# Kernel optimization log

Hardware: AMD Instinct MI355X
Metric: run time of the kernel (lower is better)

The kernel has to match this reference:

```python
import jax, jax.numpy as jnp
import numpy as np


def _layernorm(x, g, b, eps=1e-5):
    mu = jnp.mean(x, axis=-1, keepdims=True)
    var = jnp.mean(jnp.square(x - mu), axis=-1, keepdims=True)
    return (x - mu) * jax.lax.rsqrt(var + eps) * g + b


def setup_inputs() -> dict:
    key = jax.random.key(0)
    ks = jax.random.split(key, 8)
    dim, ctx_dim, heads, dim_head = 256, 256, 8, 64
    inner = heads * dim_head
    s = 0.02
    return {
        "x": jax.random.normal(ks[0], (4, dim, 64, 64), jnp.float32),
        "y": jax.random.normal(ks[1], (4, 1024, ctx_dim), jnp.float32),
        "ln_x_g": jnp.ones((dim,), jnp.float32),
        "ln_x_b": jnp.zeros((dim,), jnp.float32),
        "ln_y_g": jnp.ones((ctx_dim,), jnp.float32),
        "ln_y_b": jnp.zeros((ctx_dim,), jnp.float32),
        "Wq": jax.random.normal(ks[2], (dim, inner), jnp.float32) * s,
        "Wk": jax.random.normal(ks[3], (ctx_dim, inner), jnp.float32) * s,
        "Wv": jax.random.normal(ks[4], (ctx_dim, inner), jnp.float32) * s,
        "bv": jnp.zeros((inner,), jnp.float32),
        "Wo": jax.random.normal(ks[5], (inner, dim), jnp.float32) * s,
        "bo": jnp.zeros((dim,), jnp.float32),
    }


def reference(x, y, ln_x_g, ln_x_b, ln_y_g, ln_y_b, Wq, Wk, Wv, bv, Wo, bo):
    heads, dim_head = 8, 64
    b, c = x.shape[:2]
    # channel_last=False path: [b, c, H, W] -> [b, n, c]
    xn = x.reshape(b, c, -1).swapaxes(1, 2)
    xn = _layernorm(xn, ln_x_g, ln_x_b)          # note: x is reassigned in torch code
    yn = _layernorm(y, ln_y_g, ln_y_b)
    q = xn @ Wq                                   # [b, n, h*d]
    k = yn @ Wk                                   # [b, m, h*d]
    v = yn @ Wv + bv                              # [b, m, h*d]

    def split_heads(t):
        B, N, _ = t.shape
        return t.reshape(B, N, heads, dim_head).transpose(0, 2, 1, 3)  # [b, h, n, d]

    q, k, v = split_heads(q), split_heads(k), split_heads(v)
    attn = jnp.einsum("bhid,bhjd->bhij", q, k) * (dim_head ** -0.5)
    attn = jax.nn.softmax(attn, axis=-1)
    out = jnp.einsum("bhij,bhjd->bhid", attn, v)  # [b, h, n, d]
    out = out.transpose(0, 2, 1, 3).reshape(b, -1, heads * dim_head)
    out = out @ Wo + bo
    return xn + out  # residual with layernormed x (faithful to source)
```

## Files before the change

kernel.cpp:

```cpp
#include <hip/hip_runtime.h>
#include <hip/hip_bf16.h>
#include <cstddef>
#include <cstdint>

#define BATCH 4
#define CDIM 256
#define HW 4096
#define MCTX 1024
#define CTX 256
#define HEADS 8
#define DHEAD 64
#define INNER 512

typedef __attribute__((ext_vector_type(8))) short bf16x8;
typedef __attribute__((ext_vector_type(4))) float f32x4;
typedef __attribute__((ext_vector_type(16))) float f32x16;

static __device__ __forceinline__ ushort f2bf(float f) {
  __hip_bfloat16 h = __float2bfloat16(f);
  return *reinterpret_cast<ushort*>(&h);
}

static __device__ __forceinline__ void gload16(const void* g, void* l) {
  __builtin_amdgcn_global_load_lds(
      (const __attribute__((address_space(1))) void*)(uintptr_t)g,
      (__attribute__((address_space(3))) void*)(uint32_t)(uintptr_t)l,
      16, 0, 0);
}

static __device__ __forceinline__ void ln_x_body(
    const float* __restrict__ x, const float* __restrict__ g,
    const float* __restrict__ bta, float* __restrict__ xn,
    ushort* __restrict__ xnbf, int blk) {
  const int bi = blk / (HW / 32);
  const int n0 = (blk % (HW / 32)) * 32;
  __shared__ float xt[32][257];
  __shared__ float smu[32], srs[32];
  const int t = threadIdx.x;
  const float* xb = x + (size_t)bi * CDIM * HW;
  {
    const int cr = t >> 3;
    const int n4 = (t & 7) * 4;
    #pragma unroll
    for (int pass = 0; pass < 8; ++pass) {
      const int c = pass * 32 + cr;
      float4 v = *(const float4*)(xb + (size_t)c * HW + n0 + n4);
      xt[n4 + 0][c] = v.x; xt[n4 + 1][c] = v.y;
      xt[n4 + 2][c] = v.z; xt[n4 + 3][c] = v.w;
    }
  }
  __syncthreads();
  const int col = t >> 3, j = t & 7;
  float s = 0.f, ss = 0.f;
  #pragma unroll
  for (int c = j; c < CDIM; c += 8) {
    float v = xt[col][c];
    s += v; ss += v * v;
  }
  #pragma unroll
  for (int off = 1; off < 8; off <<= 1) {
    s += __shfl_xor(s, off);
    ss += __shfl_xor(ss, off);
  }
  if (j == 0) {
    float mu = s * (1.f / CDIM);
    smu[col] = mu;
    srs[col] = rsqrtf(ss * (1.f / CDIM) - mu * mu + 1e-5f);
  }
  __syncthreads();
  const float gv = g[t], bvv = bta[t];
  float* xnb = xn + ((size_t)bi * HW + n0) * CDIM;
  ushort* xbb = xnbf + ((size_t)bi * HW + n0) * CDIM;
  #pragma unroll 4
  for (int n = 0; n < 32; ++n) {
    float val = (xt[n][t] - smu[n]) * srs[n] * gv + bvv;
    xnb[(size_t)n * CDIM + t] = val;
    xbb[(size_t)n * CDIM + t] = f2bf(val);
  }
}

static __device__ __forceinline__ void ln_y_body(
    const float* __restrict__ y, const float* __restrict__ g,
    const float* __restrict__ bta, ushort* __restrict__ ynbf, int blk) {
  const int row = blk * 4 + (threadIdx.x >> 6);
  const int t = threadIdx.x & 63;
  float4 v = ((const float4*)(y + (size_t)row * CTX))[t];
  float s = v.x + v.y + v.z + v.w;
  float ss = v.x * v.x + v.y * v.y + v.z * v.z + v.w * v.w;
  #pragma unroll
  for (int off = 1; off < 64; off <<= 1) {
    s += __shfl_xor(s, off);
    ss += __shfl_xor(ss, off);
  }
  float mu = s * (1.f / CTX);
  float rs = rsqrtf(ss * (1.f / CTX) - mu * mu + 1e-5f);
  float4 gv = ((const float4*)g)[t];
  float4 b4 = ((const float4*)bta)[t];
  ushort4 ob;
  ob.x = f2bf((v.x - mu) * rs * gv.x + b4.x);
  ob.y = f2bf((v.y - mu) * rs * gv.y + b4.y);
  ob.z = f2bf((v.z - mu) * rs * gv.z + b4.z);
  ob.w = f2bf((v.w - mu) * rs * gv.w + b4.w);
  *(ushort4*)(ynbf + (size_t)row * CTX + t * 4) = ob;
}

static __device__ __forceinline__ void wprep_body(
    const float* __restrict__ W, ushort* __restrict__ Wt, int K, int N,
    int bx, int by) {
  __shared__ ushort T[64][65];
  const int k0 = by * 64, n0 = bx * 64;
  const int t = threadIdx.x;
  #pragma unroll
  for (int rr = 0; rr < 4; ++rr) {
    int row = rr * 16 + (t >> 4);
    int c = (t & 15) * 4;
    float4 wv = *(const float4*)(W + (size_t)(k0 + row) * N + n0 + c);
    T[row][c + 0] = f2bf(wv.x); T[row][c + 1] = f2bf(wv.y);
    T[row][c + 2] = f2bf(wv.z); T[row][c + 3] = f2bf(wv.w);
  }
  __syncthreads();
  #pragma unroll
  for (int rr = 0; rr < 4; ++rr) {
    int nrow = rr * 16 + (t >> 4);
    int kc = (t & 15) * 4;
    ushort4 o;
    o.x = T[kc + 0][nrow]; o.y = T[kc + 1][nrow];
    o.z = T[kc + 2][nrow]; o.w = T[kc + 3][nrow];
    *(ushort4*)(Wt + (size_t)(n0 + nrow) * K + k0 + kc) = o;
  }
}

__global__ __launch_bounds__(256) void prep_kernel(
    const float* __restrict__ x, const float* __restrict__ ln_xg,
    const float* __restrict__ ln_xb, float* __restrict__ xn,
    ushort* __restrict__ xnbf,
    const float* __restrict__ y, const float* __restrict__ ln_yg,
    const float* __restrict__ ln_yb, ushort* __restrict__ ynbf,
    const float* __restrict__ Wq, const float* __restrict__ Wk,
    const float* __restrict__ Wv, const float* __restrict__ Wo,
    ushort* __restrict__ wtq, ushort* __restrict__ wtk,
    ushort* __restrict__ wtv, ushort* __restrict__ wto) {
  const int id = blockIdx.x;
  if (id < 512) {
    ln_x_body(x, ln_xg, ln_xb, xn, xnbf, id);
  } else if (id < 1536) {
    ln_y_body(y, ln_yg, ln_yb, ynbf, id - 512);
  } else {
    const int r = id - 1536;
    const int z = r >> 5, rem = r & 31;
    const int bx = rem & 7, by = rem >> 3;
    if (z < 3) {
      const float* W = (z == 0) ? Wq : (z == 1) ? Wk : Wv;
      ushort* Wt = (z == 0) ? wtq : (z == 1) ? wtk : wtv;
      wprep_body(W, Wt, 256, 512, bx, by);
    } else {
      wprep_body(Wo, wto, 512, 256, bx & 3, by * 2 + (bx >> 2));
    }
  }
}

template <bool F32_RES_OUT>
static __device__ __forceinline__ void gemm_body(
    const ushort* __restrict__ A, const ushort* __restrict__ Bt,
    const float* __restrict__ bias, const float* __restrict__ res,
    void* __restrict__ Cout, ushort* __restrict__ vt_out,
    int M, int N, int K, float scale, int m0, int n0) {
  __shared__ ushort As[128 * 64];
  __shared__ ushort Bs[128 * 64];
  const int t = threadIdx.x;
  const int l = t & 63, w = t >> 6;
  const int lq = l & 15, lg = l >> 4;
  const int wr = w >> 1, wc = w & 1;
  f32x4 acc[4][4];
  #pragma unroll
  for (int mt = 0; mt < 4; ++mt)
    #pragma unroll
    for (int nt = 0; nt < 4; ++nt)
      #pragma unroll
      for (int e = 0; e < 4; ++e) acc[mt][nt][e] = 0.f;
  const int srow = w * 8 + (l >> 3);
  const int scol = ((l & 7) ^ (l >> 3)) * 8;
  const ushort* pA = A + (size_t)(m0 + srow) * K + scol;
  const ushort* pB = Bt + (size_t)(n0 + srow) * K + scol;
  const int dbase = w * 512;
  for (int k0 = 0; k0 < K; k0 += 64) {
    if (k0) __syncthreads();
    #pragma unroll
    for (int i = 0; i < 4; ++i) {
      gload16(pA + (size_t)(i * 32) * K + k0, &As[i * 2048 + dbase]);
      gload16(pB + (size_t)(i * 32) * K + k0, &Bs[i * 2048 + dbase]);
    }
    __syncthreads();
    #pragma unroll
    for (int ks = 0; ks < 2; ++ks) {
      bf16x8 af[4], bfr[4];
      #pragma unroll
      for (int mt = 0; mt < 4; ++mt) {
        const int R = wr * 64 + mt * 16 + lq;
        af[mt] = *(const bf16x8*)(
            &As[R * 64 + ((ks * 32 + lg * 8) ^ ((R & 7) * 8))]);
      }
      #pragma unroll
      for (int nt = 0; nt < 4; ++nt) {
        const int R = wc * 64 + nt * 16 + lq;
        bfr[nt] = *(const bf16x8*)(
            &Bs[R * 64 + ((ks * 32 + lg * 8) ^ ((R & 7) * 8))]);
      }
      #pragma unroll
      for (int mt = 0; mt < 4; ++mt)
        #pragma unroll
        for (int nt = 0; nt < 4; ++nt)
          acc[mt][nt] = __builtin_amdgcn_mfma_f32_16x16x32_bf16(
              af[mt], bfr[nt], acc[mt][nt], 0, 0, 0);
    }
  }
  #pragma unroll
  for (int nt = 0; nt < 4; ++nt) {
    const int colc = n0 + wc * 64 + nt * 16 + lq;
    const float bcol = bias ? bias[colc] : 0.f;
    #pragma unroll
    for (int mt = 0; mt < 4; ++mt) {
      #pragma unroll
      for (int i = 0; i < 4; ++i) {
        const size_t row = (size_t)(m0 + wr * 64 + mt * 16 + lg * 4 + i);
        float v = acc[mt][nt][i] * scale + bcol;
        if (vt_out) {
          vt_out[(size_t)((((row >> 10) * 8 + (colc >> 6)) << 6) + (colc & 63)) * MCTX
                 + (row & (MCTX - 1))] = f2bf(v);
        } else if (F32_RES_OUT) {
          ((float*)Cout)[row * N + colc] = v + res[row * N + colc];
        } else {
          ((ushort*)Cout)[row * N + colc] = f2bf(v);
        }
      }
    }
  }
}

__global__ __launch_bounds__(256) void qkv_kernel(
    const ushort* __restrict__ xnbf, const ushort* __restrict__ ynbf,
    const ushort* __restrict__ wtq, const ushort* __restrict__ wtk,
    const ushort* __restrict__ wtv, const float* __restrict__ bv,
    ushort* __restrict__ qbf, ushort* __restrict__ kbf,
    ushort* __restrict__ vtb) {
  const int id = blockIdx.x;
  if (id < 512) {
    gemm_body<false>(xnbf, wtq, nullptr, nullptr, qbf, nullptr,
                     16384, 512, 256, 0.1803368801111204f,
                     (id >> 2) * 128, (id & 3) * 128);
  } else if (id < 640) {
    const int i2 = id - 512;
    gemm_body<false>(ynbf, wtk, nullptr, nullptr, kbf, nullptr,
                     4096, 512, 256, 1.f, (i2 >> 2) * 128, (i2 & 3) * 128);
  } else {
    const int i2 = id - 640;
    gemm_body<false>(ynbf, wtv, bv, nullptr, nullptr, vtb,
                     4096, 512, 256, 1.f, (i2 >> 2) * 128, (i2 & 3) * 128);
  }
}

template <bool F32_RES_OUT>
__global__ __launch_bounds__(256) void mfma_gemm(
    const ushort* __restrict__ A, const ushort* __restrict__ Bt,
    const float* __restrict__ bias, const float* __restrict__ res,
    void* __restrict__ Cout, int M, int N, int K, float scale) {
  gemm_body<F32_RES_OUT>(A, Bt, bias, res, Cout, nullptr, M, N, K, scale,
                         blockIdx.y * 128, blockIdx.x * 128);
}

__global__ __launch_bounds__(512, 4) void attn_mfma(
    const ushort* __restrict__ q, const ushort* __restrict__ k,
    const ushort* __restrict__ vt, ushort* __restrict__ ao) {
  const int bid = blockIdx.x + 16 * (blockIdx.y + 8 * blockIdx.z);
  const int swz = (bid & 7) * 64 + (bid >> 3);
  const int bi = swz >> 7;
  const int h = (swz >> 4) & 7;
  const int n0 = (swz & 15) * 256;
  const int tile0 = (bid & 3) << 2;
  __shared__ ushort Ks[2][64 * 64];
  __shared__ ushort Vs[2][64 * 64];
  const int t = threadIdx.x;
  const int l = t & 63, w = t >> 6;
  const int lq32 = l & 31, hi = l >> 5;

  bf16x8 bq[4];
  {
    const size_t qrow = (size_t)(bi * HW + n0 + w * 32 + lq32);
    #pragma unroll
    for (int ds = 0; ds < 4; ++ds)
      bq[ds] = *(const bf16x8*)(q + qrow * INNER + h * DHEAD + ds * 16 + hi * 8);
  }

  float m_run = -1e30f, l_run = 0.f;
  f32x16 oacc[2];
  #pragma unroll
  for (int dt = 0; dt < 2; ++dt)
    #pragma unroll
    for (int e = 0; e < 16; ++e) oacc[dt][e] = 0.f;

  const int rr = t >> 3, cc = (t & 7) * 8;
  const ushort* kptr = k + (size_t)(bi * MCTX + rr) * INNER + h * DHEAD + cc;
  const ushort* vptr = vt + (size_t)((bi * HEADS + h) * 64 + rr) * MCTX + cc;
  const int sidx = (rr * 64 + cc) ^ ((rr & 7) << 3);

  {
    const int ms = tile0 << 6;
    uint4 k0v = *(const uint4*)(kptr + (size_t)ms * INNER);
    uint4 v0v = *(const uint4*)(vptr + ms);
    *(uint4*)(&Ks[0][sidx]) = k0v;
    *(uint4*)(&Vs[0][sidx]) = v0v;
  }
  __syncthreads();

  #pragma unroll 2
  for (int it = 0; it < 16; ++it) {
    const int buf = it & 1;
    const bool more = (it + 1) < 16;
    const int mnext = ((tile0 + it + 1) & 15) << 6;
    uint4 kpre{}, vpre{};
    if (more) {
      kpre = *(const uint4*)(kptr + (size_t)mnext * INNER);
      vpre = *(const uint4*)(vptr + mnext);
    }
    f32x16 sc[2];
    #pragma unroll
    for (int kt = 0; kt < 2; ++kt)
      #pragma unroll
      for (int e = 0; e < 16; ++e) sc[kt][e] = 0.f;
    __builtin_amdgcn_s_setprio(1);
    #pragma unroll
    for (int kt = 0; kt < 2; ++kt) {
      #pragma unroll
      for (int ds = 0; ds < 4; ++ds) {
        const int krow = kt * 32 + lq32;
        bf16x8 ak = *(const bf16x8*)(
            &Ks[buf][(krow * 64 + ds * 16 + hi * 8) ^ ((krow & 7) << 3)]);
        sc[kt] = __builtin_amdgcn_mfma_f32_32x32x16_bf16(ak, bq[ds], sc[kt], 0, 0, 0);
      }
    }
    __builtin_amdgcn_s_setprio(0);
    f32x16 mx;
    #pragma unroll
    for (int e = 0; e < 16; ++e) mx[e] = fmaxf(sc[0][e], sc[1][e]);
    #pragma unroll
    for (int e = 0; e < 8; ++e) mx[e] = fmaxf(mx[e], mx[e + 8]);
    #pragma unroll
    for (int e = 0; e < 4; ++e) mx[e] = fmaxf(mx[e], mx[e + 4]);
    float mloc = fmaxf(fmaxf(mx[0], mx[1]), fmaxf(mx[2], mx[3]));
    mloc = fmaxf(mloc, __shfl_xor(mloc, 32));
    if (!__all((int)(mloc - m_run <= 8.f))) {
      const float mnew = fmaxf(m_run, mloc);
      const float corr = __builtin_amdgcn_exp2f(m_run - mnew);
      l_run *= corr;
      m_run = mnew;
      #pragma unroll
      for (int r = 0; r < 16; ++r) {
        const int qrow = (r & 3) + 8 * (r >> 2) + 4 * hi;
        float ci = __shfl(corr, qrow);
        oacc[0][r] *= ci; oacc[1][r] *= ci;
      }
    }
    #pragma unroll
    for (int kt = 0; kt < 2; ++kt)
      #pragma unroll
      for (int e = 0; e < 16; ++e)
        sc[kt][e] = __builtin_amdgcn_exp2f(sc[kt][e] - m_run);
    f32x16 s16;
    #pragma unroll
    for (int e = 0; e < 16; ++e) s16[e] = sc[0][e] + sc[1][e];
    #pragma unroll
    for (int e = 0; e < 8; ++e) s16[e] += s16[e + 8];
    #pragma unroll
    for (int e = 0; e < 4; ++e) s16[e] += s16[e + 4];
    float psum = (s16[0] + s16[1]) + (s16[2] + s16[3]);
    psum += __shfl_xor(psum, 32);
    l_run += psum;
    bf16x8 pafr[4];
    #pragma unroll
    for (int kt = 0; kt < 2; ++kt) {
      uint wa[4], wb[4];
      #pragma unroll
      for (int r4 = 0; r4 < 4; ++r4) {
        wa[r4] = (uint)f2bf(sc[kt][4 * r4]) | ((uint)f2bf(sc[kt][4 * r4 + 1]) << 16);
        wb[r4] = (uint)f2bf(sc[kt][4 * r4 + 2]) | ((uint)f2bf(sc[kt][4 * r4 + 3]) << 16);
      }
      #pragma unroll
      for (int p2 = 0; p2 < 2; ++p2) {
        uint Sa = wa[2 * p2], Da = wa[2 * p2 + 1];
        uint Sb = wb[2 * p2], Db = wb[2 * p2 + 1];
        asm volatile("v_permlane32_swap_b32 %0, %1" : "+v"(Da), "+v"(Sa));
        asm volatile("v_permlane32_swap_b32 %0, %1" : "+v"(Db), "+v"(Sb));
        uint4 fr;
        fr.x = Sa; fr.y = Sb; fr.z = Da; fr.w = Db;
        pafr[kt * 2 + p2] = *reinterpret_cast<bf16x8*>(&fr);
      }
    }
    if (more) {
      *(uint4*)(&Ks[buf ^ 1][sidx]) = kpre;
      *(uint4*)(&Vs[buf ^ 1][sidx]) = vpre;
    }
    __builtin_amdgcn_s_setprio(1);
    #pragma unroll
    for (int dt = 0; dt < 2; ++dt) {
      const int vrow = dt * 32 + lq32;
      #pragma unroll
      for (int kt16 = 0; kt16 < 4; ++kt16) {
        bf16x8 vb = *(const bf16x8*)(
            &Vs[buf][(vrow * 64 + kt16 * 16 + hi * 8) ^ ((vrow & 7) << 3)]);
        oacc[dt] = __builtin_amdgcn_mfma_f32_32x32x16_bf16(pafr[kt16], vb, oacc[dt], 0, 0, 0);
      }
    }
    __builtin_amdgcn_s_setprio(0);
    __syncthreads();
  }
  const float rl = 1.f / l_run;
  #pragma unroll
  for (int r = 0; r < 16; ++r) {
    const int qrow = (r & 3) + 8 * (r >> 2) + 4 * hi;
    float li = __shfl(rl, qrow);
    const size_t row = (size_t)(bi * HW + n0 + w * 32 + qrow);
    ao[row * INNER + h * DHEAD + lq32] = f2bf(oacc[0][r] * li);
    ao[row * INNER + h * DHEAD + 32 + lq32] = f2bf(oacc[1][r] * li);
  }
}

extern "C" void kernel_launch(void* const* d_in, const int* in_sizes, int n_in,
                              void* d_out, int out_size, void* d_ws, size_t ws_size,
                              hipStream_t stream) {
  const float* x     = (const float*)d_in[0];
  const float* y     = (const float*)d_in[1];
  const float* ln_xg = (const float*)d_in[2];
  const float* ln_xb = (const float*)d_in[3];
  const float* ln_yg = (const float*)d_in[4];
  const float* ln_yb = (const float*)d_in[5];
  const float* Wq    = (const float*)d_in[6];
  const float* Wk    = (const float*)d_in[7];
  const float* Wv    = (const float*)d_in[8];
  const float* bv    = (const float*)d_in[9];
  const float* Wo    = (const float*)d_in[10];
  const float* bo    = (const float*)d_in[11];
  float* out = (float*)d_out;

  char* p = (char*)d_ws;
  float*  xn   = (float*)p;  p += (size_t)16384 * 256 * 4;
  ushort* xnbf = (ushort*)p; p += (size_t)16384 * 256 * 2;
  ushort* ynbf = (ushort*)p; p += (size_t)4096 * 256 * 2;
  ushort* wtq  = (ushort*)p; p += (size_t)512 * 256 * 2;
  ushort* wtk  = (ushort*)p; p += (size_t)512 * 256 * 2;
  ushort* wtv  = (ushort*)p; p += (size_t)512 * 256 * 2;
  ushort* wto  = (ushort*)p; p += (size_t)256 * 512 * 2;
  ushort* qbf  = (ushort*)p; p += (size_t)16384 * 512 * 2;
  ushort* kbf  = (ushort*)p; p += (size_t)4096 * 512 * 2;
  ushort* vtb  = (ushort*)p; p += (size_t)4096 * 512 * 2;
  ushort* aobf = (ushort*)p; p += (size_t)16384 * 512 * 2;

  prep_kernel<<<dim3(512 + 1024 + 128), 256, 0, stream>>>(
      x, ln_xg, ln_xb, xn, xnbf, y, ln_yg, ln_yb, ynbf,
      Wq, Wk, Wv, Wo, wtq, wtk, wtv, wto);
  qkv_kernel<<<dim3(768), 256, 0, stream>>>(
      xnbf, ynbf, wtq, wtk, wtv, bv, qbf, kbf, vtb);
  attn_mfma<<<dim3(HW / 256, HEADS, BATCH), 512, 0, stream>>>(qbf, kbf, vtb, aobf);
  mfma_gemm<true><<<dim3(2, 128), 256, 0, stream>>>(
      aobf, wto, bo, xn, out, 16384, 256, 512, 1.f);
}
```

Baseline: 104.3 us.

## Process two query tiles per attention wave and add dedicated 64-row output GEMM

The attention kernel now has each wave handle 64 query rows as two 32-row groups that share each K/V tile read from LDS. This halves the grid and the K/V global and LDS traffic per query, and the second group's softmax can overlap with the first group's MFMA work. The cost is roughly double the accumulator registers, so launch bounds drop from 4 to 2 blocks per SM. The output projection gets its own 64x128-tile kernel using 16x16x32 MFMAs, which doubles its block count for better occupancy on a narrow N=256 GEMM.

After: 105.3 us. Within noise of the previous version (+0.9%).

```diff
diff --git a/kernel.cpp b/kernel.cpp
--- a/kernel.cpp
+++ b/kernel.cpp
@@ -259,23 +259,84 @@
   }
 }
 
-template <bool F32_RES_OUT>
-__global__ __launch_bounds__(256) void mfma_gemm(
+__global__ __launch_bounds__(256) void ao_gemm_kernel(
     const ushort* __restrict__ A, const ushort* __restrict__ Bt,
     const float* __restrict__ bias, const float* __restrict__ res,
-    void* __restrict__ Cout, int M, int N, int K, float scale) {
-  gemm_body<F32_RES_OUT>(A, Bt, bias, res, Cout, nullptr, M, N, K, scale,
-                         blockIdx.y * 128, blockIdx.x * 128);
-}
-
-__global__ __launch_bounds__(512, 4) void attn_mfma(
+    float* __restrict__ out) {
+  __shared__ ushort As[64 * 64];
+  __shared__ ushort Bs[128 * 64];
+  const int t = threadIdx.x;
+  const int l = t & 63, w = t >> 6;
+  const int lq = l & 15, lg = l >> 4;
+  const int wr = w >> 1, wc = w & 1;
+  const int m0 = blockIdx.y * 64, n0 = blockIdx.x * 128;
+  f32x4 acc[2][4];
+  #pragma unroll
+  for (int mt = 0; mt < 2; ++mt)
+    #pragma unroll
+    for (int nt = 0; nt < 4; ++nt)
+      #pragma unroll
+      for (int e = 0; e < 4; ++e) acc[mt][nt][e] = 0.f;
+  const int srow = w * 8 + (l >> 3);
+  const int scol = ((l & 7) ^ (l >> 3)) * 8;
+  const ushort* pA = A + (size_t)(m0 + srow) * INNER + scol;
+  const ushort* pB = Bt + (size_t)(n0 + srow) * INNER + scol;
+  const int dbase = w * 512;
+  for (int k0 = 0; k0 < INNER; k0 += 64) {
+    if (k0) __syncthreads();
+    #pragma unroll
+    for (int i = 0; i < 2; ++i)
+      gload16(pA + (size_t)(i * 32) * INNER + k0, &As[i * 2048 + dbase]);
+    #pragma unroll
+    for (int i = 0; i < 4; ++i)
+      gload16(pB + (size_t)(i * 32) * INNER + k0, &Bs[i * 2048 + dbase]);
+    __syncthreads();
+    #pragma unroll
+    for (int ks = 0; ks < 2; ++ks) {
+      bf16x8 af[2], bfr[4];
+      #pragma unroll
+      for (int mt = 0; mt < 2; ++mt) {
+        const int R = wr * 32 + mt * 16 + lq;
+        af[mt] = *(const bf16x8*)(
+            &As[R * 64 + ((ks * 32 + lg * 8) ^ ((R & 7) * 8))]);
+      }
+      #pragma unroll
+      for (int nt = 0; nt < 4; ++nt) {
+        const int R = wc * 64 + nt * 16 + lq;
+        bfr[nt] = *(const bf16x8*)(
+            &Bs[R * 64 + ((ks * 32 + lg * 8) ^ ((R & 7) * 8))]);
+      }
+      #pragma unroll
+      for (int mt = 0; mt < 2; ++mt)
+        #pragma unroll
+        for (int nt = 0; nt < 4; ++nt)
+          acc[mt][nt] = __builtin_amdgcn_mfma_f32_16x16x32_bf16(
+              af[mt], bfr[nt], acc[mt][nt], 0, 0, 0);
+    }
+  }
+  #pragma unroll
+  for (int nt = 0; nt < 4; ++nt) {
+    const int colc = n0 + wc * 64 + nt * 16 + lq;
+    const float bcol = bias[colc];
+    #pragma unroll
+    for (int mt = 0; mt < 2; ++mt) {
+      #pragma unroll
+      for (int i = 0; i < 4; ++i) {
+        const size_t row = (size_t)(m0 + wr * 32 + mt * 16 + lg * 4 + i);
+        out[row * CDIM + colc] = acc[mt][nt][i] + bcol + res[row * CDIM + colc];
+      }
+    }
+  }
+}
+
+__global__ __launch_bounds__(512, 2) void attn_mfma(
     const ushort* __restrict__ q, const ushort* __restrict__ k,
     const ushort* __restrict__ vt, ushort* __restrict__ ao) {
-  const int bid = blockIdx.x + 16 * (blockIdx.y + 8 * blockIdx.z);
-  const int swz = (bid & 7) * 64 + (bid >> 3);
-  const int bi = swz >> 7;
-  const int h = (swz >> 4) & 7;
-  const int n0 = (swz & 15) * 256;
+  const int bid = blockIdx.x + 8 * (blockIdx.y + 8 * blockIdx.z);
+  const int swz = (bid & 7) * 32 + (bid >> 3);
+  const int bi = swz >> 6;
+  const int h = (swz >> 3) & 7;
+  const int n0 = (swz & 7) * 512;
   const int tile0 = (bid & 3) << 2;
   __shared__ ushort Ks[2][64 * 64];
   __shared__ ushort Vs[2][64 * 64];
@@ -283,20 +344,23 @@
   const int l = t & 63, w = t >> 6;
   const int lq32 = l & 31, hi = l >> 5;
 
-  bf16x8 bq[4];
+  bf16x8 bq0[4], bq1[4];
   {
-    const size_t qrow = (size_t)(bi * HW + n0 + w * 32 + lq32);
-    #pragma unroll
-    for (int ds = 0; ds < 4; ++ds)
-      bq[ds] = *(const bf16x8*)(q + qrow * INNER + h * DHEAD + ds * 16 + hi * 8);
-  }
-
-  float m_run = -1e30f, l_run = 0.f;
-  f32x16 oacc[2];
+    const size_t qr0 = (size_t)(bi * HW + n0 + w * 64 + lq32);
+    const size_t qr1 = qr0 + 32;
+    #pragma unroll
+    for (int ds = 0; ds < 4; ++ds) {
+      bq0[ds] = *(const bf16x8*)(q + qr0 * INNER + h * DHEAD + ds * 16 + hi * 8);
+      bq1[ds] = *(const bf16x8*)(q + qr1 * INNER + h * DHEAD + ds * 16 + hi * 8);
+    }
+  }
+
+  float m_run0 = -1e30f, l_run0 = 0.f, m_run1 = -1e30f, l_run1 = 0.f;
+  f32x16 oacc0[2], oacc1[2];
   #pragma unroll
   for (int dt = 0; dt < 2; ++dt)
     #pragma unroll
-    for (int e = 0; e < 16; ++e) oacc[dt][e] = 0.f;
+    for (int e = 0; e < 16; ++e) { oacc0[dt][e] = 0.f; oacc1[dt][e] = 0.f; }
 
   const int rr = t >> 3, cc = (t & 7) * 8;
   const ushort* kptr = k + (size_t)(bi * MCTX + rr) * INNER + h * DHEAD + cc;
@@ -311,6 +375,65 @@
     *(uint4*)(&Vs[0][sidx]) = v0v;
   }
   __syncthreads();
+
+  auto softmax_group = [&](f32x16 (&scg)[2], float& mr, float& lr,
+                           f32x16 (&oa)[2], bf16x8 (&paf)[4]) {
+    f32x16 mx;
+    #pragma unroll
+    for (int e = 0; e < 16; ++e) mx[e] = fmaxf(scg[0][e], scg[1][e]);
+    #pragma unroll
+    for (int e = 0; e < 8; ++e) mx[e] = fmaxf(mx[e], mx[e + 8]);
+    #pragma unroll
+    for (int e = 0; e < 4; ++e) mx[e] = fmaxf(mx[e], mx[e + 4]);
+    float mloc = fmaxf(fmaxf(mx[0], mx[1]), fmaxf(mx[2], mx[3]));
+    mloc = fmaxf(mloc, __shfl_xor(mloc, 32));
+    if (!__all((int)(mloc - mr <= 8.f))) {
+      const float mnew = fmaxf(mr, mloc);
+      const float corr = __builtin_amdgcn_exp2f(mr - mnew);
+      lr *= corr;
+      mr = mnew;
+      #pragma unroll
+      for (int r = 0; r < 16; ++r) {
+        const int qrow = (r & 3) + 8 * (r >> 2) + 4 * hi;
+        float ci = __shfl(corr, qrow);
+        oa[0][r] *= ci; oa[1][r] *= ci;
+      }
+    }
+    #pragma unroll
+    for (int kt = 0; kt < 2; ++kt)
+      #pragma unroll
+      for (int e = 0; e < 16; ++e)
+        scg[kt][e] = __builtin_amdgcn_exp2f(scg[kt][e] - mr);
+    f32x16 s16;
+    #pragma unroll
+    for (int e = 0; e < 16; ++e) s16[e] = scg[0][e] + scg[1][e];
+    #pragma unroll
+    for (int e = 0; e < 8; ++e) s16[e] += s16[e + 8];
+    #pragma unroll
+    for (int e = 0; e < 4; ++e) s16[e] += s16[e + 4];
+    float psum = (s16[0] + s16[1]) + (s16[2] + s16[3]);
+    psum += __shfl_xor(psum, 32);
+    lr += psum;
+    #pragma unroll
+    for (int kt = 0; kt < 2; ++kt) {
+      uint wa[4], wb[4];
+      #pragma unroll
+      for (int r4 = 0; r4 < 4; ++r4) {
+        wa[r4] = (uint)f2bf(scg[kt][4 * r4]) | ((uint)f2bf(scg[kt][4 * r4 + 1]) << 16);
+        wb[r4] = (uint)f2bf(scg[kt][4 * r4 + 2]) | ((uint)f2bf(scg[kt][4 * r4 + 3]) << 16);
+      }
+      #pragma unroll
+      for (int p2 = 0; p2 < 2; ++p2) {
+        uint Sa = wa[2 * p2], Da = wa[2 * p2 + 1];
+        uint Sb = wb[2 * p2], Db = wb[2 * p2 + 1];
+        asm volatile("v_permlane32_swap_b32 %0, %1" : "+v"(Da), "+v"(Sa));
+        asm volatile("v_permlane32_swap_b32 %0, %1" : "+v"(Db), "+v"(Sb));
+        uint4 fr;
+        fr.x = Sa; fr.y = Sb; fr.z = Da; fr.w = Db;
+        paf[kt * 2 + p2] = *reinterpret_cast<bf16x8*>(&fr);
+      }
+    }
+  };
 
   #pragma unroll 2
   for (int it = 0; it < 16; ++it) {
@@ -322,11 +445,11 @@
       kpre = *(const uint4*)(kptr + (size_t)mnext * INNER);
       vpre = *(const uint4*)(vptr + mnext);
     }
-    f32x16 sc[2];
+    f32x16 sc0[2], sc1[2];
     #pragma unroll
     for (int kt = 0; kt < 2; ++kt)
       #pragma unroll
-      for (int e = 0; e < 16; ++e) sc[kt][e] = 0.f;
+      for (int e = 0; e < 16; ++e) { sc0[kt][e] = 0.f; sc1[kt][e] = 0.f; }
     __builtin_amdgcn_s_setprio(1);
     #pragma unroll
     for (int kt = 0; kt < 2; ++kt) {
@@ -335,70 +458,18 @@
         const int krow = kt * 32 + lq32;
         bf16x8 ak = *(const bf16x8*)(
             &Ks[buf][(krow * 64 + ds * 16 + hi * 8) ^ ((krow & 7) << 3)]);
-        sc[kt] = __builtin_amdgcn_mfma_f32_32x32x16_bf16(ak, bq[ds], sc[kt], 0, 0, 0);
+        sc0[kt] = __builtin_amdgcn_mfma_f32_32x32x16_bf16(ak, bq0[ds], sc0[kt], 0, 0, 0);
+        sc1[kt] = __builtin_amdgcn_mfma_f32_32x32x16_bf16(ak, bq1[ds], sc1[kt], 0, 0, 0);
       }
     }
     __builtin_amdgcn_s_setprio(0);
-    f32x16 mx;
-    #pragma unroll
-    for (int e = 0; e < 16; ++e) mx[e] = fmaxf(sc[0][e], sc[1][e]);
-    #pragma unroll
-    for (int e = 0; e < 8; ++e) mx[e] = fmaxf(mx[e], mx[e + 8]);
-    #pragma unroll
-    for (int e = 0; e < 4; ++e) mx[e] = fmaxf(mx[e], mx[e + 4]);
-    float mloc = fmaxf(fmaxf(mx[0], mx[1]), fmaxf(mx[2], mx[3]));
-    mloc = fmaxf(mloc, __shfl_xor(mloc, 32));
-    if (!__all((int)(mloc - m_run <= 8.f))) {
-      const float mnew = fmaxf(m_run, mloc);
-      const float corr = __builtin_amdgcn_exp2f(m_run - mnew);
-      l_run *= corr;
-      m_run = mnew;
-      #pragma unroll
-      for (int r = 0; r < 16; ++r) {
-        const int qrow = (r & 3) + 8 * (r >> 2) + 4 * hi;
-        float ci = __shfl(corr, qrow);
-        oacc[0][r] *= ci; oacc[1][r] *= ci;
-      }
-    }
-    #pragma unroll
-    for (int kt = 0; kt < 2; ++kt)
-      #pragma unroll
-      for (int e = 0; e < 16; ++e)
-        sc[kt][e] = __builtin_amdgcn_exp2f(sc[kt][e] - m_run);
-    f32x16 s16;
-    #pragma unroll
-    for (int e = 0; e < 16; ++e) s16[e] = sc[0][e] + sc[1][e];
-    #pragma unroll
-    for (int e = 0; e < 8; ++e) s16[e] += s16[e + 8];
-    #pragma unroll
-    for (int e = 0; e < 4; ++e) s16[e] += s16[e + 4];
-    float psum = (s16[0] + s16[1]) + (s16[2] + s16[3]);
-    psum += __shfl_xor(psum, 32);
-    l_run += psum;
-    bf16x8 pafr[4];
-    #pragma unroll
-    for (int kt = 0; kt < 2; ++kt) {
-      uint wa[4], wb[4];
-      #pragma unroll
-      for (int r4 = 0; r4 < 4; ++r4) {
-        wa[r4] = (uint)f2bf(sc[kt][4 * r4]) | ((uint)f2bf(sc[kt][4 * r4 + 1]) << 16);
-        wb[r4] = (uint)f2bf(sc[kt][4 * r4 + 2]) | ((uint)f2bf(sc[kt][4 * r4 + 3]) << 16);
-      }
-      #pragma unroll
-      for (int p2 = 0; p2 < 2; ++p2) {
-        uint Sa = wa[2 * p2], Da = wa[2 * p2 + 1];
-        uint Sb = wb[2 * p2], Db = wb[2 * p2 + 1];
-        asm volatile("v_permlane32_swap_b32 %0, %1" : "+v"(Da), "+v"(Sa));
-        asm volatile("v_permlane32_swap_b32 %0, %1" : "+v"(Db), "+v"(Sb));
-        uint4 fr;
-        fr.x = Sa; fr.y = Sb; fr.z = Da; fr.w = Db;
-        pafr[kt * 2 + p2] = *reinterpret_cast<bf16x8*>(&fr);
-      }
-    }
+    bf16x8 pa0[4], pa1[4];
+    softmax_group(sc0, m_run0, l_run0, oacc0, pa0);
     if (more) {
       *(uint4*)(&Ks[buf ^ 1][sidx]) = kpre;
       *(uint4*)(&Vs[buf ^ 1][sidx]) = vpre;
     }
+    softmax_group(sc1, m_run1, l_run1, oacc1, pa1);
     __builtin_amdgcn_s_setprio(1);
     #pragma unroll
     for (int dt = 0; dt < 2; ++dt) {
@@ -407,20 +478,27 @@
       for (int kt16 = 0; kt16 < 4; ++kt16) {
         bf16x8 vb = *(const bf16x8*)(
             &Vs[buf][(vrow * 64 + kt16 * 16 + hi * 8) ^ ((vrow & 7) << 3)]);
-        oacc[dt] = __builtin_amdgcn_mfma_f32_32x32x16_bf16(pafr[kt16], vb, oacc[dt], 0, 0, 0);
+        oacc0[dt] = __builtin_amdgcn_mfma_f32_32x32x16_bf16(pa0[kt16], vb, oacc0[dt], 0, 0, 0);
+        oacc1[dt] = __builtin_amdgcn_mfma_f32_32x32x16_bf16(pa1[kt16], vb, oacc1[dt], 0, 0, 0);
       }
     }
     __builtin_amdgcn_s_setprio(0);
     __syncthreads();
   }
-  const float rl = 1.f / l_run;
-  #pragma unroll
-  for (int r = 0; r < 16; ++r) {
-    const int qrow = (r & 3) + 8 * (r >> 2) + 4 * hi;
-    float li = __shfl(rl, qrow);
-    const size_t row = (size_t)(bi * HW + n0 + w * 32 + qrow);
-    ao[row * INNER + h * DHEAD + lq32] = f2bf(oacc[0][r] * li);
-    ao[row * INNER + h * DHEAD + 32 + lq32] = f2bf(oacc[1][r] * li);
+  {
+    const float rl0 = 1.f / l_run0, rl1 = 1.f / l_run1;
+    #pragma unroll
+    for (int r = 0; r < 16; ++r) {
+      const int qrow = (r & 3) + 8 * (r >> 2) + 4 * hi;
+      const float li0 = __shfl(rl0, qrow);
+      const float li1 = __shfl(rl1, qrow);
+      const size_t row0 = (size_t)(bi * HW + n0 + w * 64 + qrow);
+      const size_t row1 = row0 + 32;
+      ao[row0 * INNER + h * DHEAD + lq32] = f2bf(oacc0[0][r] * li0);
+      ao[row0 * INNER + h * DHEAD + 32 + lq32] = f2bf(oacc0[1][r] * li0);
+      ao[row1 * INNER + h * DHEAD + lq32] = f2bf(oacc1[0][r] * li1);
+      ao[row1 * INNER + h * DHEAD + 32 + lq32] = f2bf(oacc1[1][r] * li1);
+    }
   }
 }
 
@@ -459,7 +537,6 @@
       Wq, Wk, Wv, Wo, wtq, wtk, wtv, wto);
   qkv_kernel<<<dim3(768), 256, 0, stream>>>(
       xnbf, ynbf, wtq, wtk, wtv, bv, qbf, kbf, vtb);
-  attn_mfma<<<dim3(HW / 256, HEADS, BATCH), 512, 0, stream>>>(qbf, kbf, vtb, aobf);
-  mfma_gemm<true><<<dim3(2, 128), 256, 0, stream>>>(
-      aobf, wto, bo, xn, out, 16384, 256, 512, 1.f);
-}
+  attn_mfma<<<dim3(HW / 512, HEADS, BATCH), 512, 0, stream>>>(qbf, kbf, vtb, aobf);
+  ao_gemm_kernel<<<dim3(2, 256), 256, 0, stream>>>(aobf, wto, bo, xn, out);
+}
```
